# Kernel tuning notes

Hardware: AMD Instinct MI355X
Metric: run time of the kernel (lower is better)

## Reference

```python
import jax, jax.numpy as jnp
import numpy as np

D_MODEL = 768
N_HEADS = 12
D_K = D_MODEL // N_HEADS
B, S = 2, 4096


def setup_inputs() -> dict:
    key = jax.random.key(0)
    ks = jax.random.split(key, 12)
    s_in = 1.0 / np.sqrt(D_MODEL)
    inp = {
        "Q": jax.random.normal(ks[0], (B, S, D_MODEL), jnp.float32),
        "K": jax.random.normal(ks[1], (B, S, D_MODEL), jnp.float32),
        "V": jax.random.normal(ks[2], (B, S, D_MODEL), jnp.float32),
        # nn.Linear weights are [out, in]; applied as x @ W.T + b
        "Wq": jax.random.normal(ks[3], (D_MODEL, D_MODEL), jnp.float32) * s_in,
        "bq": jax.random.normal(ks[4], (D_MODEL,), jnp.float32) * s_in,
        "Wk": jax.random.normal(ks[5], (D_MODEL, D_MODEL), jnp.float32) * s_in,
        "bk": jax.random.normal(ks[6], (D_MODEL,), jnp.float32) * s_in,
        "Wv": jax.random.normal(ks[7], (D_MODEL, D_MODEL), jnp.float32) * s_in,
        "bv": jax.random.normal(ks[8], (D_MODEL,), jnp.float32) * s_in,
        "Wo": jax.random.normal(ks[9], (D_MODEL, D_MODEL), jnp.float32) * s_in,
        "bo": jax.random.normal(ks[10], (D_MODEL,), jnp.float32) * s_in,
    }
    return inp


def _split_heads(x):
    b, s, _ = x.shape
    return x.reshape(b, s, N_HEADS, D_K).transpose(0, 2, 1, 3)  # [b,h,s,dk]


def reference(Q, K, V, Wq, bq, Wk, bk, Wv, bv, Wo, bo):
    q = _split_heads(Q @ Wq.T + bq)
    k = _split_heads(K @ Wk.T + bk)
    v = _split_heads(V @ Wv.T + bv)
    scale = 1.0 / np.sqrt(D_K).astype(np.float32)
    scores = jnp.einsum("bhqd,bhkd->bhqk", q, k) * scale  # [B,H,S,S]
    attn = jax.nn.softmax(scores, axis=-1)
    out = jnp.einsum("bhqk,bhkd->bhqd", attn, v)
    out = out.transpose(0, 2, 1, 3).reshape(Q.shape[0], Q.shape[1], D_MODEL)
    return out @ Wo.T + bo
```

## Files before the change

kernel.cpp:

```cpp
#include <hip/hip_runtime.h>
#include <hip/hip_bf16.h>

typedef __attribute__((ext_vector_type(8))) short short8;
typedef __attribute__((ext_vector_type(4))) float f32x4;
typedef __attribute__((ext_vector_type(4))) unsigned short ushort4v;

static __device__ __forceinline__ unsigned short f2bf(float f) {
  unsigned u = __float_as_uint(f);
  unsigned r = (u + 0x7fffu + ((u >> 16) & 1u)) >> 16;
  return (unsigned short)r;
}
static __device__ __forceinline__ short8 pack8(float4 a, float4 b) {
  short8 r;
  r[0] = (short)f2bf(a.x); r[1] = (short)f2bf(a.y);
  r[2] = (short)f2bf(a.z); r[3] = (short)f2bf(a.w);
  r[4] = (short)f2bf(b.x); r[5] = (short)f2bf(b.y);
  r[6] = (short)f2bf(b.z); r[7] = (short)f2bf(b.w);
  return r;
}

template <int CTRL>
static __device__ __forceinline__ float fmax_dpp(float x) {
  int t = __builtin_amdgcn_update_dpp(__float_as_int(x), __float_as_int(x),
                                      CTRL, 0xF, 0xF, true);
  return fmaxf(x, __int_as_float(t));
}
static __device__ __forceinline__ float max16_dpp(float x) {
  x = fmax_dpp<0xB1>(x);
  x = fmax_dpp<0x4E>(x);
  x = fmax_dpp<0x141>(x);
  x = fmax_dpp<0x140>(x);
  return x;
}

template<int XF32, int OUTF32>
__device__ __forceinline__ void gemm128(
    const void* Xp, const float* W, const float* bias,
    void* outp, float scale, int vt_mode, int bm, int bn)
{
  __shared__ unsigned short Als[128 * 32];
  __shared__ unsigned short Bls[128 * 32];

  const int tid = threadIdx.x;
  const int wave = tid >> 6, lane = tid & 63;
  const int g = lane >> 4, lo = lane & 15;
  const int wr = wave >> 1, wc = wave & 1;
  const int m0 = bm * 128, n0 = bn * 128;

  const f32x4 vzero = {0.f, 0.f, 0.f, 0.f};
  f32x4 acc[4][4];
#pragma unroll
  for (int m = 0; m < 4; ++m)
#pragma unroll
    for (int n = 0; n < 4; ++n) acc[m][n] = vzero;

  const int arow = tid >> 1;
  const int acol = (tid & 1) * 16;
  const float* Af = nullptr;
  const unsigned short* Ab = nullptr;
  if constexpr (XF32) Af = (const float*)Xp + (size_t)(m0 + arow) * 768 + acol;
  else                Ab = (const unsigned short*)Xp + (size_t)(m0 + arow) * 768 + acol;
  const float* Brow = W + (size_t)(n0 + arow) * 768 + acol;

  for (int k0 = 0; k0 < 768; k0 += 32) {
    short8 va0, va1;
    if constexpr (XF32) {
      float4 f0 = *(const float4*)(Af + k0);
      float4 f1 = *(const float4*)(Af + k0 + 4);
      float4 f2 = *(const float4*)(Af + k0 + 8);
      float4 f3 = *(const float4*)(Af + k0 + 12);
      va0 = pack8(f0, f1);
      va1 = pack8(f2, f3);
    } else {
      va0 = *(const short8*)(Ab + k0);
      va1 = *(const short8*)(Ab + k0 + 8);
    }
    float4 g0 = *(const float4*)(Brow + k0);
    float4 g1 = *(const float4*)(Brow + k0 + 4);
    float4 g2 = *(const float4*)(Brow + k0 + 8);
    float4 g3 = *(const float4*)(Brow + k0 + 12);
    short8 vb0 = pack8(g0, g1);
    short8 vb1 = pack8(g2, g3);

    __syncthreads();
    *(short8*)(Als + arow * 32 + acol)     = va0;
    *(short8*)(Als + arow * 32 + acol + 8) = va1;
    *(short8*)(Bls + arow * 32 + acol)     = vb0;
    *(short8*)(Bls + arow * 32 + acol + 8) = vb1;
    __syncthreads();

    short8 af[4], bf[4];
#pragma unroll
    for (int m = 0; m < 4; ++m)
      af[m] = *(const short8*)(Als + (wr * 64 + m * 16 + lo) * 32 + g * 8);
#pragma unroll
    for (int n = 0; n < 4; ++n)
      bf[n] = *(const short8*)(Bls + (wc * 64 + n * 16 + lo) * 32 + g * 8);
#pragma unroll
    for (int m = 0; m < 4; ++m)
#pragma unroll
      for (int n = 0; n < 4; ++n)
        acc[m][n] = __builtin_amdgcn_mfma_f32_16x16x32_bf16(af[m], bf[n], acc[m][n], 0, 0, 0);
  }

#pragma unroll
  for (int n = 0; n < 4; ++n) {
    const int ncol = n0 + wc * 64 + n * 16 + lo;
    const float bb = bias[ncol];
#pragma unroll
    for (int m = 0; m < 4; ++m) {
      const int rowb = m0 + wr * 64 + m * 16 + g * 4;
      if constexpr (OUTF32) {
        float* out = (float*)outp;
#pragma unroll
        for (int r = 0; r < 4; ++r)
          out[(size_t)(rowb + r) * 768 + ncol] = (acc[m][n][r] + bb) * scale;
      } else {
        unsigned short* out = (unsigned short*)outp;
        if (!vt_mode) {
#pragma unroll
          for (int r = 0; r < 4; ++r)
            out[(size_t)(rowb + r) * 768 + ncol] = f2bf((acc[m][n][r] + bb) * scale);
        } else {
          const int b = rowb >> 12, s = rowb & 4095;
          const int hh = ncol >> 6, d = ncol & 63;
          ushort4v pk;
#pragma unroll
          for (int r = 0; r < 4; ++r) pk[r] = f2bf((acc[m][n][r] + bb) * scale);
          *(ushort4v*)(out + (((size_t)b * 12 + hh) * 64 + d) * 4096 + s) = pk;
        }
      }
    }
  }
}

__global__ __launch_bounds__(256, 2) void qkv_proj(
    const float* __restrict__ Qi, const float* __restrict__ Ki,
    const float* __restrict__ Vi,
    const float* __restrict__ Wq, const float* __restrict__ bq,
    const float* __restrict__ Wk, const float* __restrict__ bk,
    const float* __restrict__ Wv, const float* __restrict__ bv,
    unsigned short* __restrict__ qo, unsigned short* __restrict__ ko,
    unsigned short* __restrict__ vto)
{
  const int z = blockIdx.z;
  const float* X = (z == 0) ? Qi : (z == 1) ? Ki : Vi;
  const float* W = (z == 0) ? Wq : (z == 1) ? Wk : Wv;
  const float* bb = (z == 0) ? bq : (z == 1) ? bk : bv;
  unsigned short* out = (z == 0) ? qo : (z == 1) ? ko : vto;
  const float scale = (z == 0) ? 0.18033688011f : 1.0f;
  gemm128<1, 0>(X, W, bb, out, scale, (z == 2) ? 1 : 0, blockIdx.x, blockIdx.y);
}

__global__ __launch_bounds__(256, 2) void out_proj(
    const unsigned short* __restrict__ X, const float* __restrict__ W,
    const float* __restrict__ bias, float* __restrict__ out)
{
  gemm128<0, 1>(X, W, bias, out, 1.0f, 0, blockIdx.x, blockIdx.y);
}

__global__ __launch_bounds__(512, 6) void attn_fwd(
    const unsigned short* qw, const unsigned short* __restrict__ kw,
    const unsigned short* __restrict__ vtw, unsigned short* ow)
{
  __shared__ unsigned short Kls[64 * 64];
  __shared__ unsigned short Vls[64 * 64];
  __shared__ unsigned short Pls[8 * 16 * 72];

  const int tid = threadIdx.x, wave = tid >> 6, lane = tid & 63;
  const int g = lane >> 4, lo = lane & 15;
  const int bh = blockIdx.y, b = bh / 12, hh = bh % 12;
  const int q0 = blockIdx.x * 128 + wave * 16;

  short8 aq[2];
#pragma unroll
  for (int s = 0; s < 2; ++s)
    aq[s] = *(const short8*)(qw + (size_t)(b * 4096 + q0 + lo) * 768
                             + hh * 64 + s * 32 + g * 8);

  const f32x4 vzero = {0.f, 0.f, 0.f, 0.f};
  float mx[4];
  f32x4 lacc = vzero;
  f32x4 oacc[4];
#pragma unroll
  for (int r = 0; r < 4; ++r) mx[r] = -1e30f;
#pragma unroll
  for (int n = 0; n < 4; ++n) oacc[n] = vzero;

  short8 bone;
#pragma unroll
  for (int j = 0; j < 8; ++j) bone[j] = (short)0x3F80;

  unsigned short* Pw = Pls + wave * (16 * 72);
  char* Kb = (char*)Kls;
  char* Vb = (char*)Vls;

  const int srow = tid >> 3;
  const int sc = tid & 7;
  const unsigned short* krow = kw + ((size_t)b * 4096 + srow) * 768 + hh * 64 + sc * 8;
  const unsigned short* vrow = vtw + ((size_t)bh * 64 + srow) * 4096 + sc * 8;
  const int sdst = srow * 128 + ((sc * 16) ^ ((srow & 7) << 4));

  short8 kl = *(const short8*)(krow);
  short8 vl = *(const short8*)(vrow);

  for (int kv0 = 0; kv0 < 4096; kv0 += 64) {
    asm volatile("s_waitcnt lgkmcnt(0)" ::: "memory");
    __builtin_amdgcn_s_barrier();
    *(short8*)(Kb + sdst) = kl;
    *(short8*)(Vb + sdst) = vl;
    if (kv0 + 64 < 4096) {
      kl = *(const short8*)(krow + (size_t)(kv0 + 64) * 768);
      vl = *(const short8*)(vrow + (kv0 + 64));
    }
    asm volatile("s_waitcnt lgkmcnt(0)" ::: "memory");
    __builtin_amdgcn_s_barrier();
    __builtin_amdgcn_sched_barrier(0);

    f32x4 sa[4];
#pragma unroll
    for (int n = 0; n < 4; ++n) {
      const int row = n * 16 + lo;
      const int rsw = (row & 7) << 4;
      short8 bk0 = *(const short8*)(Kb + row * 128 + ((g * 16) ^ rsw));
      short8 bk1 = *(const short8*)(Kb + row * 128 + ((64 + g * 16) ^ rsw));
      f32x4 t = vzero;
      t = __builtin_amdgcn_mfma_f32_16x16x32_bf16(aq[0], bk0, t, 0, 0, 0);
      t = __builtin_amdgcn_mfma_f32_16x16x32_bf16(aq[1], bk1, t, 0, 0, 0);
      sa[n] = t;
    }

#pragma unroll
    for (int r = 0; r < 4; ++r) {
      float pm = fmaxf(fmaxf(sa[0][r], sa[1][r]), fmaxf(sa[2][r], sa[3][r]));
      pm = max16_dpp(pm);
      if (pm > mx[r] + 8.f) {
        const float fr = __builtin_amdgcn_exp2f(mx[r] - pm);
        mx[r] = pm;
        lacc[r] *= fr;
#pragma unroll
        for (int nd = 0; nd < 4; ++nd) oacc[nd][r] *= fr;
      }
#pragma unroll
      for (int n = 0; n < 4; ++n)
        Pw[(g * 4 + r) * 72 + n * 16 + lo] =
            f2bf(__builtin_amdgcn_exp2f(sa[n][r] - mx[r]));
    }

    short8 ap0 = *(const short8*)((char*)Pw + lo * 144 + g * 16);
    short8 ap1 = *(const short8*)((char*)Pw + lo * 144 + 64 + g * 16);
#pragma unroll
    for (int nd = 0; nd < 4; ++nd) {
      const int row = nd * 16 + lo;
      const int rsw = (row & 7) << 4;
      short8 bv0 = *(const short8*)(Vb + row * 128 + ((g * 16) ^ rsw));
      short8 bv1 = *(const short8*)(Vb + row * 128 + ((64 + g * 16) ^ rsw));
      oacc[nd] = __builtin_amdgcn_mfma_f32_16x16x32_bf16(ap0, bv0, oacc[nd], 0, 0, 0);
      oacc[nd] = __builtin_amdgcn_mfma_f32_16x16x32_bf16(ap1, bv1, oacc[nd], 0, 0, 0);
    }
    lacc = __builtin_amdgcn_mfma_f32_16x16x32_bf16(ap0, bone, lacc, 0, 0, 0);
    lacc = __builtin_amdgcn_mfma_f32_16x16x32_bf16(ap1, bone, lacc, 0, 0, 0);
  }

#pragma unroll
  for (int r = 0; r < 4; ++r) {
    const float inv = 1.f / lacc[r];
    const size_t rowoff = (size_t)(b * 4096 + q0 + g * 4 + r) * 768 + hh * 64;
#pragma unroll
    for (int nd = 0; nd < 4; ++nd)
      ow[rowoff + nd * 16 + lo] = f2bf(oacc[nd][r] * inv);
  }
}

extern "C" void kernel_launch(void* const* d_in, const int* in_sizes, int n_in,
                              void* d_out, int out_size, void* d_ws, size_t ws_size,
                              hipStream_t stream) {
  (void)in_sizes; (void)n_in; (void)out_size; (void)ws_size;
  const float* Qi = (const float*)d_in[0];
  const float* Ki = (const float*)d_in[1];
  const float* Vi = (const float*)d_in[2];
  const float* Wq = (const float*)d_in[3];
  const float* bq = (const float*)d_in[4];
  const float* Wk = (const float*)d_in[5];
  const float* bk = (const float*)d_in[6];
  const float* Wv = (const float*)d_in[7];
  const float* bv = (const float*)d_in[8];
  const float* Wo = (const float*)d_in[9];
  const float* bo = (const float*)d_in[10];

  unsigned short* ws = (unsigned short*)d_ws;
  const size_t NTOK = 8192u * 768u;
  unsigned short* qw  = ws;
  unsigned short* vtw = ws + NTOK;
  unsigned short* kwp = (unsigned short*)d_out;

  qkv_proj<<<dim3(64, 6, 3), 256, 0, stream>>>(Qi, Ki, Vi, Wq, bq, Wk, bk,
                                               Wv, bv, qw, kwp, vtw);
  attn_fwd<<<dim3(32, 24, 1), 512, 0, stream>>>(qw, kwp, vtw, qw);
  out_proj<<<dim3(64, 6, 1), 256, 0, stream>>>(qw, Wo, bo, (float*)d_out);
}
```

Baseline: 297.6 us.

## Pre-convert projection weights to bf16 and truncate softmax probabilities

Adds a small kernel that converts all four weight matrices to bf16 once per call into workspace, so the GEMMs load bf16 weights directly instead of loading fp32 and converting inside every tile. This halves weight load traffic and removes the repeated conversion from the inner GEMM loop. Also switches fp32→bf16 packing to the HIP intrinsic, and replaces round-to-nearest of the softmax probabilities with plain truncation. The costs are an extra kernel launch and slightly less accurate probabilities.

```diff
diff --git a/kernel.cpp b/kernel.cpp
--- a/kernel.cpp
+++ b/kernel.cpp
@@ -10,12 +10,16 @@
   unsigned r = (u + 0x7fffu + ((u >> 16) & 1u)) >> 16;
   return (unsigned short)r;
 }
+static __device__ __forceinline__ unsigned short f2bf_fast(float f) {
+  __hip_bfloat16 h = __float2bfloat16(f);
+  return *reinterpret_cast<unsigned short*>(&h);
+}
 static __device__ __forceinline__ short8 pack8(float4 a, float4 b) {
   short8 r;
-  r[0] = (short)f2bf(a.x); r[1] = (short)f2bf(a.y);
-  r[2] = (short)f2bf(a.z); r[3] = (short)f2bf(a.w);
-  r[4] = (short)f2bf(b.x); r[5] = (short)f2bf(b.y);
-  r[6] = (short)f2bf(b.z); r[7] = (short)f2bf(b.w);
+  r[0] = (short)f2bf_fast(a.x); r[1] = (short)f2bf_fast(a.y);
+  r[2] = (short)f2bf_fast(a.z); r[3] = (short)f2bf_fast(a.w);
+  r[4] = (short)f2bf_fast(b.x); r[5] = (short)f2bf_fast(b.y);
+  r[6] = (short)f2bf_fast(b.z); r[7] = (short)f2bf_fast(b.w);
   return r;
 }
 
@@ -33,9 +37,25 @@
   return x;
 }
 
+__global__ __launch_bounds__(256) void cvt_w4(
+    const float* __restrict__ w0, const float* __restrict__ w1,
+    const float* __restrict__ w2, const float* __restrict__ w3,
+    unsigned short* __restrict__ o)
+{
+  const int z = blockIdx.y;
+  const float* src = (z == 0) ? w0 : (z == 1) ? w1 : (z == 2) ? w2 : w3;
+  unsigned short* dst = o + (size_t)z * 589824;
+  const int i = blockIdx.x * 256 + threadIdx.x;
+  float4 f = ((const float4*)src)[i];
+  ushort4v v;
+  v[0] = f2bf_fast(f.x); v[1] = f2bf_fast(f.y);
+  v[2] = f2bf_fast(f.z); v[3] = f2bf_fast(f.w);
+  ((ushort4v*)dst)[i] = v;
+}
+
 template<int XF32, int OUTF32>
 __device__ __forceinline__ void gemm128(
-    const void* Xp, const float* W, const float* bias,
+    const void* Xp, const unsigned short* Wb, const float* bias,
     void* outp, float scale, int vt_mode, int bm, int bn)
 {
   __shared__ unsigned short Als[128 * 32];
@@ -60,7 +80,7 @@
   const unsigned short* Ab = nullptr;
   if constexpr (XF32) Af = (const float*)Xp + (size_t)(m0 + arow) * 768 + acol;
   else                Ab = (const unsigned short*)Xp + (size_t)(m0 + arow) * 768 + acol;
-  const float* Brow = W + (size_t)(n0 + arow) * 768 + acol;
+  const unsigned short* Brow = Wb + (size_t)(n0 + arow) * 768 + acol;
 
   for (int k0 = 0; k0 < 768; k0 += 32) {
     short8 va0, va1;
@@ -75,12 +95,8 @@
       va0 = *(const short8*)(Ab + k0);
       va1 = *(const short8*)(Ab + k0 + 8);
     }
-    float4 g0 = *(const float4*)(Brow + k0);
-    float4 g1 = *(const float4*)(Brow + k0 + 4);
-    float4 g2 = *(const float4*)(Brow + k0 + 8);
-    float4 g3 = *(const float4*)(Brow + k0 + 12);
-    short8 vb0 = pack8(g0, g1);
-    short8 vb1 = pack8(g2, g3);
+    short8 vb0 = *(const short8*)(Brow + k0);
+    short8 vb1 = *(const short8*)(Brow + k0 + 8);
 
     __syncthreads();
     *(short8*)(Als + arow * 32 + acol)     = va0;
@@ -137,15 +153,15 @@
 __global__ __launch_bounds__(256, 2) void qkv_proj(
     const float* __restrict__ Qi, const float* __restrict__ Ki,
     const float* __restrict__ Vi,
-    const float* __restrict__ Wq, const float* __restrict__ bq,
-    const float* __restrict__ Wk, const float* __restrict__ bk,
-    const float* __restrict__ Wv, const float* __restrict__ bv,
+    const unsigned short* __restrict__ Wq, const float* __restrict__ bq,
+    const unsigned short* __restrict__ Wk, const float* __restrict__ bk,
+    const unsigned short* __restrict__ Wv, const float* __restrict__ bv,
     unsigned short* __restrict__ qo, unsigned short* __restrict__ ko,
     unsigned short* __restrict__ vto)
 {
   const int z = blockIdx.z;
   const float* X = (z == 0) ? Qi : (z == 1) ? Ki : Vi;
-  const float* W = (z == 0) ? Wq : (z == 1) ? Wk : Wv;
+  const unsigned short* W = (z == 0) ? Wq : (z == 1) ? Wk : Wv;
   const float* bb = (z == 0) ? bq : (z == 1) ? bk : bv;
   unsigned short* out = (z == 0) ? qo : (z == 1) ? ko : vto;
   const float scale = (z == 0) ? 0.18033688011f : 1.0f;
@@ -153,7 +169,7 @@
 }
 
 __global__ __launch_bounds__(256, 2) void out_proj(
-    const unsigned short* __restrict__ X, const float* __restrict__ W,
+    const unsigned short* __restrict__ X, const unsigned short* __restrict__ W,
     const float* __restrict__ bias, float* __restrict__ out)
 {
   gemm128<0, 1>(X, W, bias, out, 1.0f, 0, blockIdx.x, blockIdx.y);
@@ -242,9 +258,11 @@
         for (int nd = 0; nd < 4; ++nd) oacc[nd][r] *= fr;
       }
 #pragma unroll
-      for (int n = 0; n < 4; ++n)
-        Pw[(g * 4 + r) * 72 + n * 16 + lo] =
-            f2bf(__builtin_amdgcn_exp2f(sa[n][r] - mx[r]));
+      for (int n = 0; n < 4; ++n) {
+        const float pv = __builtin_amdgcn_exp2f(sa[n][r] - mx[r]);
+        *(unsigned short*)((char*)Pw + (g * 4 + r) * 144 + n * 32 + lo * 2) =
+            (unsigned short)(__float_as_uint(pv) >> 16);
+      }
     }
 
     short8 ap0 = *(const short8*)((char*)Pw + lo * 144 + g * 16);
@@ -290,12 +308,19 @@
 
   unsigned short* ws = (unsigned short*)d_ws;
   const size_t NTOK = 8192u * 768u;
+  const size_t NW = 589824;
   unsigned short* qw  = ws;
   unsigned short* vtw = ws + NTOK;
+  unsigned short* wbf = ws + 2 * NTOK;
+  unsigned short* Wqc = wbf;
+  unsigned short* Wkc = wbf + NW;
+  unsigned short* Wvc = wbf + 2 * NW;
+  unsigned short* Woc = wbf + 3 * NW;
   unsigned short* kwp = (unsigned short*)d_out;
 
-  qkv_proj<<<dim3(64, 6, 3), 256, 0, stream>>>(Qi, Ki, Vi, Wq, bq, Wk, bk,
-                                               Wv, bv, qw, kwp, vtw);
+  cvt_w4<<<dim3(576, 4), 256, 0, stream>>>(Wq, Wk, Wv, Wo, wbf);
+  qkv_proj<<<dim3(64, 6, 3), 256, 0, stream>>>(Qi, Ki, Vi, Wqc, bq, Wkc, bk,
+                                               Wvc, bv, qw, kwp, vtw);
   attn_fwd<<<dim3(32, 24, 1), 512, 0, stream>>>(qw, kwp, vtw, qw);
-  out_proj<<<dim3(64, 6, 1), 256, 0, stream>>>(qw, Wo, bo, (float*)d_out);
-}
+  out_proj<<<dim3(64, 6, 1), 256, 0, stream>>>(qw, Woc, bo, (float*)d_out);
+}
```

Measured after the change: 255.3 us. -14.2%, faster.
